# Optimization experiments

Hardware: AMD Instinct MI355X
Metric: run time of the kernel (lower is better)

Reference implementation:

```python
import jax, jax.numpy as jnp
import numpy as np

WIN = 16           # window side -> L = 256
NUM_HEADS = 16
LOG_MAX = 4.605170185988092  # math.log(1/0.01)
EPS = 1e-12        # F.normalize default eps


def _rel_coords_log():
    # pair-wise log-spaced relative coordinates, shape (L*L, 2)
    coords = jnp.stack(jnp.meshgrid(jnp.arange(WIN), jnp.arange(WIN), indexing='ij'), axis=0).reshape(2, -1)
    rel = (coords[:, :, None] - coords[:, None, :]).transpose(1, 2, 0).reshape(-1, 2).astype(jnp.float32)
    return jnp.sign(rel) * jnp.log1p(jnp.abs(rel))


def _l2norm(t):
    return t / jnp.maximum(jnp.linalg.norm(t, axis=-1, keepdims=True), EPS)


def setup_inputs() -> dict:
    key = jax.random.key(0)
    ks = jax.random.split(key, 6)
    Bw, L, C = 256, WIN * WIN, 512
    return {
        'x': jax.random.normal(ks[0], (Bw, L, C), jnp.float32),
        'qkv_w': jax.random.normal(ks[1], (3 * C, C), jnp.float32) * 0.02,
        'qkv_b': jnp.zeros((3 * C,), jnp.float32),
        'proj_w': jax.random.normal(ks[2], (C, C), jnp.float32) * 0.02,
        'proj_b': jnp.zeros((C,), jnp.float32),
        'fc1_w': jax.random.normal(ks[3], (512, 2), jnp.float32) * 0.02,
        'fc1_b': jnp.zeros((512,), jnp.float32),
        'fc2_w': jax.random.normal(ks[4], (NUM_HEADS, 512), jnp.float32) * 0.02,
        'fc2_b': jnp.zeros((NUM_HEADS,), jnp.float32),
        'logit_scale': jnp.log(10.0 * jnp.ones((NUM_HEADS,), jnp.float32)),
    }


def reference(x, qkv_w, qkv_b, proj_w, proj_b, fc1_w, fc1_b, fc2_w, fc2_b, logit_scale):
    Bw, L, C = x.shape
    H = NUM_HEADS
    d = C // H
    # fused qkv projection -> (3, Bw, H, L, d)
    qkv = (x @ qkv_w.T + qkv_b).reshape(Bw, L, 3, H, d).transpose(2, 0, 3, 1, 4)
    q, k, v = qkv[0], qkv[1], qkv[2]
    # cosine attention: L2-normalized q/k, per-head learned logit scale
    attn = jnp.einsum('bhqd,bhkd->bhqk', _l2norm(q), _l2norm(k))
    scale = jnp.exp(jnp.minimum(logit_scale, LOG_MAX)).reshape(1, H, 1, 1)
    # continuous relative position bias via 2-layer MLP
    rel = _rel_coords_log()                       # (L*L, 2)
    hid = jax.nn.relu(rel @ fc1_w.T + fc1_b)      # (L*L, 512)
    bias = (hid @ fc2_w.T + fc2_b).T.reshape(H, L, L)
    attn = jax.nn.softmax(attn * scale + bias[None], axis=-1)
    out = jnp.einsum('bhqk,bhkd->bhqd', attn, v).transpose(0, 2, 1, 3).reshape(Bw, L, C)
    return out @ proj_w.T + proj_b
```

## Files before the change

kernel.cpp:

```cpp
#include <hip/hip_runtime.h>
#include <hip/hip_bf16.h>
#include <math.h>

#define WINS 16
#define LTOK 256
#define CCH  512
#define NH   16
#define DH   32
#define NBW  256
#define LOG_MAX_F 4.605170185988092f
#define EPS_F 1e-12f

typedef __attribute__((ext_vector_type(8))) short bf16x8;
typedef __attribute__((ext_vector_type(4))) float f32x4;

__device__ __forceinline__ unsigned short bf16rne(float f) {
  unsigned int u = __float_as_uint(f);
  u += 0x7fffu + ((u >> 16) & 1u);
  return (unsigned short)(u >> 16);
}
__device__ __forceinline__ float bf2f(unsigned short s) {
  return __uint_as_float(((unsigned int)s) << 16);
}

#define LGKM0 do { asm volatile("s_waitcnt lgkmcnt(0)" ::: "memory"); \
                   __builtin_amdgcn_sched_barrier(0); } while (0)

__global__ __launch_bounds__(256) void split_kernel(
    const float* __restrict__ in, unsigned short* __restrict__ out, long nElem)
{
  long total4 = nElem >> 2;
  for (long i4 = (long)blockIdx.x * 256 + threadIdx.x; i4 < total4;
       i4 += (long)gridDim.x * 256) {
    long row = i4 >> 7;
    int  kq  = ((int)i4 & 127) << 2;
    float4 a = *(const float4*)&in[(row << 9) + kq];
    unsigned int b0 = __float_as_uint(a.x), b1 = __float_as_uint(a.y);
    unsigned int b2 = __float_as_uint(a.z), b3 = __float_as_uint(a.w);
    ushort4 hi = make_ushort4((unsigned short)(b0 >> 16), (unsigned short)(b1 >> 16),
                              (unsigned short)(b2 >> 16), (unsigned short)(b3 >> 16));
    float l0 = a.x - __uint_as_float(b0 & 0xffff0000u);
    float l1 = a.y - __uint_as_float(b1 & 0xffff0000u);
    float l2 = a.z - __uint_as_float(b2 & 0xffff0000u);
    float l3 = a.w - __uint_as_float(b3 & 0xffff0000u);
    ushort4 lo = make_ushort4(bf16rne(l0), bf16rne(l1), bf16rne(l2), bf16rne(l3));
    *(ushort4*)&out[row * 1024 + kq]       = hi;
    *(ushort4*)&out[row * 1024 + 512 + kq] = lo;
  }
}

__global__ __launch_bounds__(64) void bias_mlp_kernel(
    const float* __restrict__ fc1_w, const float* __restrict__ fc1_b,
    const float* __restrict__ fc2_w, const float* __restrict__ fc2_b,
    float* __restrict__ table)
{
  const int e  = blockIdx.x;
  const int di = e / 31 - 15;
  const int dj = e % 31 - 15;
  const float rx = (di > 0 ? 1.f : (di < 0 ? -1.f : 0.f)) * log1pf(fabsf((float)di));
  const float ry = (dj > 0 ? 1.f : (dj < 0 ? -1.f : 0.f)) * log1pf(fabsf((float)dj));
  const int lane = threadIdx.x;

  float acc[NH];
#pragma unroll
  for (int h = 0; h < NH; ++h) acc[h] = 0.f;

  for (int j = lane; j < 512; j += 64) {
    float hid = fmaf(fc1_w[2*j], rx, fmaf(fc1_w[2*j+1], ry, fc1_b[j]));
    hid = fmaxf(hid, 0.f);
#pragma unroll
    for (int h = 0; h < NH; ++h) acc[h] = fmaf(fc2_w[h*512 + j], hid, acc[h]);
  }
#pragma unroll
  for (int h = 0; h < NH; ++h) {
    float v = acc[h];
    for (int off = 32; off > 0; off >>= 1) v += __shfl_down(v, off);
    if (lane == 0) table[h*961 + e] = v + fc2_b[h];
  }
}

__global__ __launch_bounds__(256) void mh_kernel(
    const float* __restrict__ table, const float* __restrict__ lscale,
    float* __restrict__ Mh)
{
  const int t = threadIdx.x, h = t >> 4, l16 = t & 15;
  float bm = -1e30f;
  for (int e = l16; e < 961; e += 16) bm = fmaxf(bm, table[h*961 + e]);
#pragma unroll
  for (int off = 1; off < 16; off <<= 1) bm = fmaxf(bm, __shfl_xor(bm, off));
  if (l16 == 0)
    Mh[h] = __expf(fminf(lscale[h], LOG_MAX_F)) + bm + 1e-3f;
}

__global__ __launch_bounds__(256) void gemm_mfma_split(
    const unsigned short* __restrict__ A,
    const unsigned short* __restrict__ B,
    const float* __restrict__ bias,
    float* __restrict__ C,
    int M, int N, int K)
{
  __shared__ unsigned short As[128 * 32];
  __shared__ unsigned short Bs[128 * 32];

  const int nwg  = gridDim.x;
  const int id   = (blockIdx.x & 7) * (nwg >> 3) + (blockIdx.x >> 3);
  const int ntls = N >> 7;
  const int mt = id / ntls, nt = id % ntls;

  const int tid  = threadIdx.x;
  const int wave = tid >> 6;
  const int lane = tid & 63;
  const int wr = wave >> 1, wc = wave & 1;
  const size_t m0 = (size_t)mt * 128, n0 = (size_t)nt * 128;
  const int K2 = 2 * K;

  f32x4 acc[4][4];
#pragma unroll
  for (int i = 0; i < 4; ++i)
#pragma unroll
    for (int j = 0; j < 4; ++j) acc[i][j] = 0.f;

  const int srow = (lane >> 2);
  const int sko  = (lane & 3) * 8;

  for (int t3 = 0; t3 < 3; ++t3) {
    const int kaB = (t3 < 2) ? 0 : K;
    const int kbB = (t3 == 1) ? K : 0;
    for (int kt = 0; kt < K; kt += 32) {
      const int ka = kaB + kt, kb = kbB + kt;
      __syncthreads();
#pragma unroll
      for (int L = 0; L < 2; ++L) {
        const int r0 = wave * 32 + L * 16;
        __builtin_amdgcn_global_load_lds(
            (const __attribute__((address_space(1))) unsigned int*)
                &A[(m0 + r0 + srow) * (size_t)K2 + ka + sko],
            (__attribute__((address_space(3))) unsigned int*)&As[r0 * 32],
            16, 0, 0);
        __builtin_amdgcn_global_load_lds(
            (const __attribute__((address_space(1))) unsigned int*)
                &B[(n0 + r0 + srow) * (size_t)K2 + kb + sko],
            (__attribute__((address_space(3))) unsigned int*)&Bs[r0 * 32],
            16, 0, 0);
      }
      asm volatile("s_waitcnt vmcnt(0)" ::: "memory");
      __syncthreads();

      const int fr = lane & 15, fk = (lane >> 4) * 8;
      bf16x8 af[4], bfr[4];
#pragma unroll
      for (int i = 0; i < 4; ++i)
        af[i] = *(const bf16x8*)&As[(wr * 64 + i * 16 + fr) * 32 + fk];
#pragma unroll
      for (int j = 0; j < 4; ++j)
        bfr[j] = *(const bf16x8*)&Bs[(wc * 64 + j * 16 + fr) * 32 + fk];
#pragma unroll
      for (int i = 0; i < 4; ++i)
#pragma unroll
        for (int j = 0; j < 4; ++j)
          acc[i][j] = __builtin_amdgcn_mfma_f32_16x16x32_bf16(
              af[i], bfr[j], acc[i][j], 0, 0, 0);
    }
  }

  const int cr = (lane >> 4) * 4, cc = lane & 15;
#pragma unroll
  for (int j = 0; j < 4; ++j) {
    const size_t col = n0 + wc * 64 + j * 16 + cc;
    const float bv = bias[col];
#pragma unroll
    for (int i = 0; i < 4; ++i) {
      const size_t rbase = m0 + wr * 64 + i * 16 + cr;
#pragma unroll
      for (int r = 0; r < 4; ++r)
        C[(rbase + r) * (size_t)N + col] = acc[i][j][r] + bv;
    }
  }
}

__global__ __launch_bounds__(256) void attn_kernel(
    const float* __restrict__ qkv,
    const float* __restrict__ table,
    const float* __restrict__ lscale,
    const float* __restrict__ Mh,
    unsigned short* __restrict__ Osp)
{
  __shared__ unsigned short Khi[256 * 40];
  __shared__ unsigned short Klo[256 * 40];
  __shared__ unsigned short Vth[32 * 264];
  __shared__ unsigned short Pql[4 * 512];
  __shared__ unsigned short btb[962];

  const int b = blockIdx.x, h = blockIdx.y, t = threadIdx.x;
  const int lane = t & 63, w = t >> 6;
  const int G = lane >> 4, ql = lane & 15;
  const float scale = __expf(fminf(lscale[h], LOG_MAX_F));
  const float Mhv = Mh[h];

  {
    const size_t rb = ((size_t)(b*LTOK + t)) * (3*CCH) + CCH + h*DH;
    float4 kr[8]; float nk = 0.f;
#pragma unroll
    for (int c = 0; c < 8; ++c) {
      kr[c] = *(const float4*)&qkv[rb + c*4];
      nk += kr[c].x*kr[c].x + kr[c].y*kr[c].y + kr[c].z*kr[c].z + kr[c].w*kr[c].w;
    }
    const float ik = 1.f / fmaxf(sqrtf(nk), EPS_F);
#pragma unroll
    for (int c = 0; c < 4; ++c) {
      float f[8] = {kr[2*c].x*ik, kr[2*c].y*ik, kr[2*c].z*ik, kr[2*c].w*ik,
                    kr[2*c+1].x*ik, kr[2*c+1].y*ik, kr[2*c+1].z*ik, kr[2*c+1].w*ik};
      bf16x8 hi, lo;
#pragma unroll
      for (int j = 0; j < 8; ++j) {
        unsigned int u = __float_as_uint(f[j]);
        hi[j] = (short)(u >> 16);
        lo[j] = (short)bf16rne(f[j] - __uint_as_float(u & 0xffff0000u));
      }
      *(bf16x8*)&Khi[t*40 + c*8] = hi;
      *(bf16x8*)&Klo[t*40 + c*8] = lo;
    }
  }
  {
    const size_t rb = ((size_t)(b*LTOK + t)) * (3*CCH) + 2*CCH + h*DH;
#pragma unroll
    for (int c = 0; c < 8; ++c) {
      float4 v = *(const float4*)&qkv[rb + c*4];
      Vth[(4*c+0)*264 + t] = bf16rne(v.x);
      Vth[(4*c+1)*264 + t] = bf16rne(v.y);
      Vth[(4*c+2)*264 + t] = bf16rne(v.z);
      Vth[(4*c+3)*264 + t] = bf16rne(v.w);
    }
  }
  for (int e = t; e < 961; e += 256) btb[e] = bf16rne(table[h*961 + e]);

  bf16x8 Qh[4], Qlr[4];
#pragma unroll
  for (int qt = 0; qt < 4; ++qt) {
    const int qrow = b*LTOK + w*64 + qt*16 + ql;
    const float* qp = &qkv[(size_t)qrow * (3*CCH) + h*DH + G*8];
    float4 a = *(const float4*)qp;
    float4 b4 = *(const float4*)(qp + 4);
    float ss = a.x*a.x + a.y*a.y + a.z*a.z + a.w*a.w
             + b4.x*b4.x + b4.y*b4.y + b4.z*b4.z + b4.w*b4.w;
    ss += __shfl_xor(ss, 16);
    ss += __shfl_xor(ss, 32);
    const float iq = scale / fmaxf(sqrtf(ss), EPS_F);
    float f[8] = {a.x*iq, a.y*iq, a.z*iq, a.w*iq, b4.x*iq, b4.y*iq, b4.z*iq, b4.w*iq};
#pragma unroll
    for (int j = 0; j < 8; ++j) {
      unsigned int u = __float_as_uint(f[j]);
      Qh[qt][j]  = (short)(u >> 16);
      Qlr[qt][j] = (short)bf16rne(f[j] - __uint_as_float(u & 0xffff0000u));
    }
  }
  __syncthreads();

  f32x4 accO[2][4];
#pragma unroll
  for (int i = 0; i < 2; ++i)
#pragma unroll
    for (int j = 0; j < 4; ++j) accO[i][j] = 0.f;
  float lsum[4] = {0.f, 0.f, 0.f, 0.f};

  const int pbase = w * 512;

  for (int kp = 0; kp < 8; ++kp) {
    bf16x8 kh[2], kl[2], vf[2];
#pragma unroll
    for (int tt = 0; tt < 2; ++tt) {
      const int krow = kp*32 + tt*16 + ql;
      kh[tt] = *(const bf16x8*)&Khi[krow*40 + G*8];
      kl[tt] = *(const bf16x8*)&Klo[krow*40 + G*8];
    }
#pragma unroll
    for (int dt = 0; dt < 2; ++dt)
      vf[dt] = *(const bf16x8*)&Vth[(dt*16 + ql)*264 + kp*32 + G*8];

#pragma unroll
    for (int qt = 0; qt < 4; ++qt) {
      f32x4 st0, st1; st0 = 0.f; st1 = 0.f;
      st0 = __builtin_amdgcn_mfma_f32_16x16x32_bf16(kl[0], Qh[qt],  st0, 0,0,0);
      st0 = __builtin_amdgcn_mfma_f32_16x16x32_bf16(kh[0], Qlr[qt], st0, 0,0,0);
      st0 = __builtin_amdgcn_mfma_f32_16x16x32_bf16(kh[0], Qh[qt],  st0, 0,0,0);
      st1 = __builtin_amdgcn_mfma_f32_16x16x32_bf16(kl[1], Qh[qt],  st1, 0,0,0);
      st1 = __builtin_amdgcn_mfma_f32_16x16x32_bf16(kh[1], Qlr[qt], st1, 0,0,0);
      st1 = __builtin_amdgcn_mfma_f32_16x16x32_bf16(kh[1], Qh[qt],  st1, 0,0,0);

      const int qg = w*64 + qt*16 + ql;
      const int qi = qg >> 4, qj = qg & 15;
      unsigned short ph[2][4];
#pragma unroll
      for (int tt = 0; tt < 2; ++tt) {
        const int ki = kp*2 + tt;
#pragma unroll
        for (int r = 0; r < 4; ++r) {
          const int kj = 4*G + r;
          const float bv = bf2f(btb[(qi - ki + 15)*31 + (qj - kj + 15)]);
          const float sv = (tt == 0) ? st0[r] : st1[r];
          const float p = __expf(sv + bv - Mhv);
          const unsigned short us = bf16rne(p);
          ph[tt][r] = us;
          lsum[qt] += bf2f(us);
        }
      }

      LGKM0;
#pragma unroll
      for (int tt = 0; tt < 2; ++tt) {
        const int chunkw = 2*tt + (G >> 1);
        const int widx = pbase + ql*32 + ((chunkw ^ (ql & 3)) * 8) + (G & 1)*4;
        *(ushort4*)&Pql[widx] = make_ushort4(ph[tt][0], ph[tt][1], ph[tt][2], ph[tt][3]);
      }
      LGKM0;

      const bf16x8 pb = *(const bf16x8*)&Pql[pbase + ql*32 + ((G ^ (ql & 3)) * 8)];
      accO[0][qt] = __builtin_amdgcn_mfma_f32_16x16x32_bf16(vf[0], pb, accO[0][qt], 0,0,0);
      accO[1][qt] = __builtin_amdgcn_mfma_f32_16x16x32_bf16(vf[1], pb, accO[1][qt], 0,0,0);
    }
  }

#pragma unroll
  for (int qt = 0; qt < 4; ++qt) {
    float lq = lsum[qt];
    lq += __shfl_xor(lq, 16);
    lq += __shfl_xor(lq, 32);
    const float inv = 1.f / fmaxf(lq, 1e-37f);
    const int qrow = b*LTOK + w*64 + qt*16 + ql;
#pragma unroll
    for (int dt = 0; dt < 2; ++dt) {
      unsigned short hv[4], lv[4];
#pragma unroll
      for (int r = 0; r < 4; ++r) {
        const float v = accO[dt][qt][r] * inv;
        const unsigned int u = __float_as_uint(v);
        hv[r] = (unsigned short)(u >> 16);
        lv[r] = bf16rne(v - __uint_as_float(u & 0xffff0000u));
      }
      unsigned short* ob = &Osp[(size_t)qrow * 1024 + h*DH + dt*16 + G*4];
      *(ushort4*)ob         = make_ushort4(hv[0], hv[1], hv[2], hv[3]);
      *(ushort4*)(ob + 512) = make_ushort4(lv[0], lv[1], lv[2], lv[3]);
    }
  }
}

extern "C" void kernel_launch(void* const* d_in, const int* in_sizes, int n_in,
                              void* d_out, int out_size, void* d_ws, size_t ws_size,
                              hipStream_t stream) {
  const float* x      = (const float*)d_in[0];
  const float* qkv_w  = (const float*)d_in[1];
  const float* qkv_b  = (const float*)d_in[2];
  const float* proj_w = (const float*)d_in[3];
  const float* proj_b = (const float*)d_in[4];
  const float* fc1_w  = (const float*)d_in[5];
  const float* fc1_b  = (const float*)d_in[6];
  const float* fc2_w  = (const float*)d_in[7];
  const float* fc2_b  = (const float*)d_in[8];
  const float* ls     = (const float*)d_in[9];
  float* out = (float*)d_out;

  const size_t FIXED   = 65536 + (size_t)1536*1024*2 + (size_t)512*1024*2;
  const size_t PER_WIN = (size_t)LTOK*(3*CCH)*4 + 2*(size_t)LTOK*1024*2;

  int CW = NBW;
  while (CW > 4 && FIXED + (size_t)CW * PER_WIN > ws_size) CW >>= 1;

  char* p = (char*)d_ws;
  float*          table   = (float*)p;          p += 65536;
  unsigned short* qkvw_s  = (unsigned short*)p; p += (size_t)1536*1024*2;
  unsigned short* projw_s = (unsigned short*)p; p += (size_t)512*1024*2;
  float*          qkvbuf  = (float*)p;          p += (size_t)CW*LTOK*(3*CCH)*4;
  unsigned short* xsplit  = (unsigned short*)p; p += (size_t)CW*LTOK*1024*2;
  unsigned short* osplit  = (unsigned short*)p;
  float*          MhPtr   = table + NH*961;

  bias_mlp_kernel<<<dim3(961), dim3(64), 0, stream>>>(fc1_w, fc1_b, fc2_w, fc2_b, table);
  mh_kernel<<<dim3(1), dim3(256), 0, stream>>>(table, ls, MhPtr);
  split_kernel<<<dim3(768), dim3(256), 0, stream>>>(qkv_w, qkvw_s, (long)1536*512);
  split_kernel<<<dim3(256), dim3(256), 0, stream>>>(proj_w, projw_s, (long)512*512);

  const int Mc = CW * LTOK;
  const long xElems = (long)Mc * CCH;
  const int splitGrid = (int)((xElems/4 + 255) / 256) > 2048 ? 2048
                        : (int)((xElems/4 + 255) / 256);

  for (int c0 = 0; c0 < NBW; c0 += CW) {
    const float* xc = x   + (size_t)c0 * LTOK * CCH;
    float*       oc = out + (size_t)c0 * LTOK * CCH;

    split_kernel<<<dim3(splitGrid), dim3(256), 0, stream>>>(xc, xsplit, xElems);

    gemm_mfma_split<<<dim3((Mc/128) * (1536/128)), dim3(256), 0, stream>>>(
        xsplit, qkvw_s, qkv_b, qkvbuf, Mc, 1536, CCH);

    attn_kernel<<<dim3(CW, NH), dim3(256), 0, stream>>>(
        qkvbuf, table, ls, MhPtr, osplit);

    gemm_mfma_split<<<dim3((Mc/128) * (512/128)), dim3(256), 0, stream>>>(
        osplit, projw_s, proj_b, oc, Mc, 512, CCH);
  }
}
```

Before: 1.162 ms.

## Fuse three split-bf16 GEMM passes into one K loop; drop attention LDS waits

The split-precision GEMM used to run three full K passes (hi*hi, hi*lo, lo*hi), reloading A and B tiles from global memory in each pass. It now loads the hi and lo tiles of A and B together in a single K loop and issues all three MFMA groups per tile, so each operand is fetched once and there are a third as many barriers. This doubles LDS use and raises register pressure from the extra fragments. Separately, the explicit lgkmcnt waits and scheduling barriers around the P write/read in attention are removed, leaving the compiler to order that LDS round trip within the wave.

```diff
diff --git a/kernel.cpp b/kernel.cpp
--- a/kernel.cpp
+++ b/kernel.cpp
@@ -22,9 +22,6 @@
 __device__ __forceinline__ float bf2f(unsigned short s) {
   return __uint_as_float(((unsigned int)s) << 16);
 }
-
-#define LGKM0 do { asm volatile("s_waitcnt lgkmcnt(0)" ::: "memory"); \
-                   __builtin_amdgcn_sched_barrier(0); } while (0)
 
 __global__ __launch_bounds__(256) void split_kernel(
     const float* __restrict__ in, unsigned short* __restrict__ out, long nElem)
@@ -99,8 +96,10 @@
     float* __restrict__ C,
     int M, int N, int K)
 {
-  __shared__ unsigned short As[128 * 32];
-  __shared__ unsigned short Bs[128 * 32];
+  __shared__ unsigned short Ah[128 * 32];
+  __shared__ unsigned short Al[128 * 32];
+  __shared__ unsigned short Bh[128 * 32];
+  __shared__ unsigned short Bl[128 * 32];
 
   const int nwg  = gridDim.x;
   const int id   = (blockIdx.x & 7) * (nwg >> 3) + (blockIdx.x >> 3);
@@ -123,44 +122,58 @@
   const int srow = (lane >> 2);
   const int sko  = (lane & 3) * 8;
 
-  for (int t3 = 0; t3 < 3; ++t3) {
-    const int kaB = (t3 < 2) ? 0 : K;
-    const int kbB = (t3 == 1) ? K : 0;
-    for (int kt = 0; kt < K; kt += 32) {
-      const int ka = kaB + kt, kb = kbB + kt;
-      __syncthreads();
-#pragma unroll
-      for (int L = 0; L < 2; ++L) {
-        const int r0 = wave * 32 + L * 16;
-        __builtin_amdgcn_global_load_lds(
-            (const __attribute__((address_space(1))) unsigned int*)
-                &A[(m0 + r0 + srow) * (size_t)K2 + ka + sko],
-            (__attribute__((address_space(3))) unsigned int*)&As[r0 * 32],
-            16, 0, 0);
-        __builtin_amdgcn_global_load_lds(
-            (const __attribute__((address_space(1))) unsigned int*)
-                &B[(n0 + r0 + srow) * (size_t)K2 + kb + sko],
-            (__attribute__((address_space(3))) unsigned int*)&Bs[r0 * 32],
-            16, 0, 0);
-      }
-      asm volatile("s_waitcnt vmcnt(0)" ::: "memory");
-      __syncthreads();
-
-      const int fr = lane & 15, fk = (lane >> 4) * 8;
-      bf16x8 af[4], bfr[4];
-#pragma unroll
-      for (int i = 0; i < 4; ++i)
-        af[i] = *(const bf16x8*)&As[(wr * 64 + i * 16 + fr) * 32 + fk];
+  for (int kt = 0; kt < K; kt += 32) {
+    __syncthreads();
+#pragma unroll
+    for (int L = 0; L < 2; ++L) {
+      const int r0 = wave * 32 + L * 16;
+      const size_t arow = (m0 + r0 + srow) * (size_t)K2;
+      const size_t brow = (n0 + r0 + srow) * (size_t)K2;
+      __builtin_amdgcn_global_load_lds(
+          (const __attribute__((address_space(1))) unsigned int*)&A[arow + kt + sko],
+          (__attribute__((address_space(3))) unsigned int*)&Ah[r0 * 32], 16, 0, 0);
+      __builtin_amdgcn_global_load_lds(
+          (const __attribute__((address_space(1))) unsigned int*)&A[arow + K + kt + sko],
+          (__attribute__((address_space(3))) unsigned int*)&Al[r0 * 32], 16, 0, 0);
+      __builtin_amdgcn_global_load_lds(
+          (const __attribute__((address_space(1))) unsigned int*)&B[brow + kt + sko],
+          (__attribute__((address_space(3))) unsigned int*)&Bh[r0 * 32], 16, 0, 0);
+      __builtin_amdgcn_global_load_lds(
+          (const __attribute__((address_space(1))) unsigned int*)&B[brow + K + kt + sko],
+          (__attribute__((address_space(3))) unsigned int*)&Bl[r0 * 32], 16, 0, 0);
+    }
+    asm volatile("s_waitcnt vmcnt(0)" ::: "memory");
+    __syncthreads();
+
+    const int fr = lane & 15, fk = (lane >> 4) * 8;
+    bf16x8 ah[4], al[4], bh[4], bl[4];
+#pragma unroll
+    for (int i = 0; i < 4; ++i) {
+      const int ra = (wr * 64 + i * 16 + fr) * 32 + fk;
+      ah[i] = *(const bf16x8*)&Ah[ra];
+      al[i] = *(const bf16x8*)&Al[ra];
+    }
+#pragma unroll
+    for (int j = 0; j < 4; ++j) {
+      const int rb = (wc * 64 + j * 16 + fr) * 32 + fk;
+      bh[j] = *(const bf16x8*)&Bh[rb];
+      bl[j] = *(const bf16x8*)&Bl[rb];
+    }
+#pragma unroll
+    for (int i = 0; i < 4; ++i)
 #pragma unroll
       for (int j = 0; j < 4; ++j)
-        bfr[j] = *(const bf16x8*)&Bs[(wc * 64 + j * 16 + fr) * 32 + fk];
-#pragma unroll
-      for (int i = 0; i < 4; ++i)
-#pragma unroll
-        for (int j = 0; j < 4; ++j)
-          acc[i][j] = __builtin_amdgcn_mfma_f32_16x16x32_bf16(
-              af[i], bfr[j], acc[i][j], 0, 0, 0);
-    }
+        acc[i][j] = __builtin_amdgcn_mfma_f32_16x16x32_bf16(ah[i], bh[j], acc[i][j], 0, 0, 0);
+#pragma unroll
+    for (int i = 0; i < 4; ++i)
+#pragma unroll
+      for (int j = 0; j < 4; ++j)
+        acc[i][j] = __builtin_amdgcn_mfma_f32_16x16x32_bf16(ah[i], bl[j], acc[i][j], 0, 0, 0);
+#pragma unroll
+    for (int i = 0; i < 4; ++i)
+#pragma unroll
+      for (int j = 0; j < 4; ++j)
+        acc[i][j] = __builtin_amdgcn_mfma_f32_16x16x32_bf16(al[i], bh[j], acc[i][j], 0, 0, 0);
   }
 
   const int cr = (lane >> 4) * 4, cc = lane & 15;
@@ -305,15 +318,12 @@
         }
       }
 
-      LGKM0;
 #pragma unroll
       for (int tt = 0; tt < 2; ++tt) {
         const int chunkw = 2*tt + (G >> 1);
         const int widx = pbase + ql*32 + ((chunkw ^ (ql & 3)) * 8) + (G & 1)*4;
         *(ushort4*)&Pql[widx] = make_ushort4(ph[tt][0], ph[tt][1], ph[tt][2], ph[tt][3]);
       }
-      LGKM0;
-
       const bf16x8 pb = *(const bf16x8*)&Pql[pbase + ql*32 + ((G ^ (ql & 3)) * 8)];
       accO[0][qt] = __builtin_amdgcn_mfma_f32_16x16x32_bf16(vf[0], pb, accO[0][qt], 0,0,0);
       accO[1][qt] = __builtin_amdgcn_mfma_f32_16x16x32_bf16(vf[1], pb, accO[1][qt], 0,0,0);
```

Result: faster. 956.4 us (-17.7%).
